# Performance work log

Measured on AMD Instinct MI355X. Metric: run time of the kernel, lower is better.

Reference implementation:

```python
import jax, jax.numpy as jnp
import numpy as np

NF4 = jnp.array([-1.0, -0.6961928009986877, -0.5250730514526367, -0.39491748809814453,
                 -0.28444138169288635, -0.18477343022823334, -0.09105003625154495, 0.0,
                 0.07958029955625534, 0.16093020141124725, 0.24611230194568634,
                 0.33791524171829224, 0.44070982933044434, 0.5626170039176941,
                 0.7229568362236023, 1.0], dtype=jnp.float32)
BLOCK_SIZE = 64
SCALING = 32.0 / 16.0  # alpha / rank


def setup_inputs() -> dict:
    key = jax.random.key(0)
    k = jax.random.split(key, 6)
    B, S, IN, OUT, R = 4, 128, 4096, 11008, 16
    n_blocks = (OUT * IN) // BLOCK_SIZE  # 704512, exact (no padding needed)
    return {
        "x": jax.random.normal(k[0], (B, S, IN), jnp.float32),
        "weight_indices": jax.random.randint(k[1], (OUT, IN), 0, 16, dtype=jnp.int32),
        "weight_scales": jax.random.uniform(k[2], (n_blocks,), jnp.float32),
        "lora_A": jax.random.normal(k[3], (IN, R), jnp.float32),
        "lora_B": jax.random.normal(k[4], (R, OUT), jnp.float32),
        "bias": jax.random.normal(k[5], (OUT,), jnp.float32),
    }


def dequantize_nf4(indices, scales, shape):
    # LUT gather then blockwise absmax scale
    w = NF4[indices.reshape(-1)]                    # [out*in]
    w = w.reshape(-1, BLOCK_SIZE) * scales[:, None]  # [n_blocks, block]
    return w.reshape(shape)                          # [out, in]


def reference(x, weight_indices, weight_scales, lora_A, lora_B, bias):
    W = dequantize_nf4(weight_indices, weight_scales, weight_indices.shape)  # [out, in]
    base = jnp.einsum("bsi,oi->bso", x, W) + bias                            # F.linear
    lora = (x @ lora_A) @ lora_B                                             # low-rank path (dropout p=0 -> identity)
    return base + lora * SCALING
```

## Files before the change

kernel.cpp:

```cpp
#include <hip/hip_runtime.h>
#include <stdint.h>

typedef __bf16 bf16x8 __attribute__((ext_vector_type(8)));
typedef float f32x4 __attribute__((ext_vector_type(4)));
typedef unsigned short ushort_t;

#define N_OUT 11008
#define K_DIM 4096
#define M_DIM 512
#define BM 256
#define BN 64
#define BK 64
#define KHALF 2048
#define NT 32

__constant__ float c_nf4[16] = {
    -1.0f, -0.6961928009986877f, -0.5250730514526367f, -0.39491748809814453f,
    -0.28444138169288635f, -0.18477343022823334f, -0.09105003625154495f, 0.0f,
    0.07958029955625534f, 0.16093020141124725f, 0.24611230194568634f,
    0.33791524171829224f, 0.44070982933044434f, 0.5626170039176941f,
    0.7229568362236023f, 1.0f};

__device__ __forceinline__ uint32_t pkbf(float lo, float hi) {
  uint32_t ul = __builtin_bit_cast(uint32_t, lo);
  uint32_t uh = __builtin_bit_cast(uint32_t, hi);
  return ((ul + 0x8000u) >> 16) | ((uh + 0x8000u) & 0xffff0000u);
}

__device__ __forceinline__ void async16(const void* g, void* l) {
  __builtin_amdgcn_global_load_lds(
      (const __attribute__((address_space(1))) void*)g,
      (__attribute__((address_space(3))) void*)l, 16, 0, 0);
}

__device__ __forceinline__ bf16x8 ldfrag(const ushort_t* p) {
  uint4 r = *reinterpret_cast<const uint4*>(p);
  return __builtin_bit_cast(bf16x8, r);
}

__device__ __forceinline__ uint32_t dq2(int a, int b, float s, const float2* lut) {
  float2 l = lut[a | (b << 4)];
  return pkbf(l.x * s, l.y * s);
}

__global__ void k_prep(const float* __restrict__ x, const float* __restrict__ lA,
                       const float* __restrict__ lB, const float* __restrict__ bias,
                       ushort_t* __restrict__ xbf, ushort_t* __restrict__ xap,
                       ushort_t* __restrict__ btp, float* __restrict__ out) {
  const int b = blockIdx.x, t = threadIdx.x;
  if (b < 1024) {
    int oc = b * 256 + t;
    int m = oc >> 9;
    int cr = oc & 511;
    int win = cr >> 3, cp = cr & 7;
    int c = cp ^ (m & 7);
    const float4* s4 = (const float4*)(x + (size_t)m * K_DIM + win * 64 + c * 8);
    float4 v0 = s4[0], v1 = s4[1];
    uint4 o;
    o.x = pkbf(v0.x, v0.y);
    o.y = pkbf(v0.z, v0.w);
    o.z = pkbf(v1.x, v1.y);
    o.w = pkbf(v1.z, v1.w);
    ((uint4*)xbf)[oc] = o;
  } else if (b < 1536) {
    __shared__ float red[256 * 17];
    int m = b - 1024;
    int ks = t * 16;
    alignas(16) float xs[16];
    const f32x4* xv = (const f32x4*)(x + (size_t)m * K_DIM + ks);
    ((f32x4*)xs)[0] = xv[0];
    ((f32x4*)xs)[1] = xv[1];
    ((f32x4*)xs)[2] = xv[2];
    ((f32x4*)xs)[3] = xv[3];
    f32x4 ac0 = 0.f, ac1 = 0.f, ac2 = 0.f, ac3 = 0.f;
#pragma unroll
    for (int kk = 0; kk < 16; ++kk) {
      float xk = xs[kk];
      const f32x4* l4 = (const f32x4*)(lA + (size_t)(ks + kk) * 16);
      ac0 += xk * l4[0];
      ac1 += xk * l4[1];
      ac2 += xk * l4[2];
      ac3 += xk * l4[3];
    }
#pragma unroll
    for (int r = 0; r < 4; ++r) {
      red[t * 17 + r] = ac0[r];
      red[t * 17 + 4 + r] = ac1[r];
      red[t * 17 + 8 + r] = ac2[r];
      red[t * 17 + 12 + r] = ac3[r];
    }
    __syncthreads();
#pragma unroll
    for (int s = 128; s >= 16; s >>= 1) {
      if (t < s)
        for (int r = 0; r < 16; ++r) red[t * 17 + r] += red[(t + s) * 17 + r];
      __syncthreads();
    }
    if (t < 32) {
      float v = 0.f;
      if (t < 16) {
        for (int p = 0; p < 16; ++p) v += red[p * 17 + t];
        v *= 2.0f;
      }
      uint32_t u = __builtin_bit_cast(uint32_t, v);
      xap[(size_t)m * 32 + t] = (ushort_t)((u + 0x8000u) >> 16);
    }
  } else if (b < 1579) {
    int o = (b - 1536) * 256 + t;
    uint32_t p[8];
#pragma unroll
    for (int j = 0; j < 8; ++j)
      p[j] = pkbf(lB[(size_t)(2 * j) * N_OUT + o], lB[(size_t)(2 * j + 1) * N_OUT + o]);
    uint4* dst = reinterpret_cast<uint4*>(btp + (size_t)o * 32);
    dst[0] = make_uint4(p[0], p[1], p[2], p[3]);
    dst[1] = make_uint4(p[4], p[5], p[6], p[7]);
    dst[2] = make_uint4(0u, 0u, 0u, 0u);
    dst[3] = make_uint4(0u, 0u, 0u, 0u);
  } else {
    int i = (b - 1579) * 256 + t;
    int col4 = i % 2752;
    ((float4*)out)[i] = ((const float4*)bias)[col4];
  }
}

__launch_bounds__(256, 3)
__global__ void k_main(const ushort_t* __restrict__ xbf, const int* __restrict__ wi,
                       const float* __restrict__ sc, const ushort_t* __restrict__ xap,
                       const ushort_t* __restrict__ btp, float* __restrict__ out) {
  __shared__ __align__(16) ushort_t lds_a[BM * BK];
  __shared__ __align__(16) ushort_t lds_b[BN * 72];
  __shared__ float2 lutp[256];

  const int t = threadIdx.x;
  const int lane = t & 63;
  const int w = t >> 6;
  const int o0 = blockIdx.x * BN;
  const int m0 = blockIdx.y * BM;
  const int kh = blockIdx.z;
  const int k0 = kh * KHALF;

  lutp[t] = make_float2(c_nf4[t & 15], c_nf4[t >> 4]);

  const int brow = t >> 2, bq = t & 3;
  const int* gb = wi + (size_t)(o0 + brow) * K_DIM + k0 + bq * 16;
  const float* gs = sc + (size_t)(o0 + brow) * 64 + kh * 32;
  ushort_t* lb = lds_b + brow * 72 + bq * 16;

  const ushort_t* ga =
      xbf + (size_t)(m0 + w * 64 + (lane >> 3)) * K_DIM + k0 + (lane & 7) * 8;
  ushort_t* la_dst = lds_a + w * 4096 + lane * 8;

  f32x4 acc[4][4];
#pragma unroll
  for (int mi = 0; mi < 4; ++mi)
#pragma unroll
    for (int ni = 0; ni < 4; ++ni) acc[mi][ni] = (f32x4){0.f, 0.f, 0.f, 0.f};

  int4 bi0 = ((const int4*)gb)[0], bi1 = ((const int4*)gb)[1];
  int4 bi2 = ((const int4*)gb)[2], bi3 = ((const int4*)gb)[3];
  float s = gs[0];
  gb += BK;
  uint4 braw;

  const ushort_t* afb = lds_a + (w * 64 + (lane & 15)) * BK;
  const int q = lane >> 4;
  const ushort_t* bfb = lds_b + (lane & 15) * 72 + q * 8;

#pragma unroll 1
  for (int kt = 0; kt < NT; ++kt) {
    __syncthreads();
    uint4 w0, w1;
    w0.x = dq2(bi0.x, bi0.y, s, lutp);
    w0.y = dq2(bi0.z, bi0.w, s, lutp);
    w0.z = dq2(bi1.x, bi1.y, s, lutp);
    w0.w = dq2(bi1.z, bi1.w, s, lutp);
    w1.x = dq2(bi2.x, bi2.y, s, lutp);
    w1.y = dq2(bi2.z, bi2.w, s, lutp);
    w1.z = dq2(bi3.x, bi3.y, s, lutp);
    w1.w = dq2(bi3.z, bi3.w, s, lutp);
    *reinterpret_cast<uint4*>(lb) = w0;
    *reinterpret_cast<uint4*>(lb + 8) = w1;
#pragma unroll
    for (int j = 0; j < 8; ++j)
      async16(ga + (size_t)j * 8 * K_DIM + kt * BK, la_dst + j * 512);
    __syncthreads();
    if (kt + 1 < NT) {
      bi0 = ((const int4*)gb)[0];
      bi1 = ((const int4*)gb)[1];
      bi2 = ((const int4*)gb)[2];
      bi3 = ((const int4*)gb)[3];
      s = gs[kt + 1];
      gb += BK;
    } else if (kh == 1) {
      braw = *reinterpret_cast<const uint4*>(btp + (size_t)(o0 + brow) * 32 + bq * 8);
    }
#pragma unroll
    for (int kc = 0; kc < 2; ++kc) {
      const int cpr = ((kc * 4 + q) ^ (lane & 7)) * 8;
      bf16x8 av[4], bv[4];
#pragma unroll
      for (int mi = 0; mi < 4; ++mi) av[mi] = ldfrag(afb + mi * 16 * BK + cpr);
#pragma unroll
      for (int ni = 0; ni < 4; ++ni) bv[ni] = ldfrag(bfb + ni * 16 * 72 + kc * 32);
#pragma unroll
      for (int mi = 0; mi < 4; ++mi)
#pragma unroll
        for (int ni = 0; ni < 4; ++ni)
          acc[mi][ni] = __builtin_amdgcn_mfma_f32_16x16x32_bf16(av[mi], bv[ni],
                                                                acc[mi][ni], 0, 0, 0);
    }
  }

  if (kh == 1) {
    __syncthreads();
    *reinterpret_cast<uint4*>(lds_b + brow * 72 + bq * 8) = braw;
#pragma unroll
    for (int j = 0; j < 4; ++j)
      async16(xap + (size_t)(m0 + w * 64 + j * 16 + (lane >> 2)) * 32 + (lane & 3) * 8,
              lds_a + w * 2048 + j * 512 + lane * 8);
    __syncthreads();
    bf16x8 av[4], bv[4];
#pragma unroll
    for (int mi = 0; mi < 4; ++mi)
      av[mi] = ldfrag(lds_a + w * 2048 + (mi * 16 + (lane & 15)) * 32 + q * 8);
#pragma unroll
    for (int ni = 0; ni < 4; ++ni)
      bv[ni] = ldfrag(lds_b + (ni * 16 + (lane & 15)) * 72 + q * 8);
#pragma unroll
    for (int mi = 0; mi < 4; ++mi)
#pragma unroll
      for (int ni = 0; ni < 4; ++ni)
        acc[mi][ni] = __builtin_amdgcn_mfma_f32_16x16x32_bf16(av[mi], bv[ni],
                                                              acc[mi][ni], 0, 0, 0);
  }

  const int cl = lane & 15, rg = q * 4;
#pragma unroll
  for (int ni = 0; ni < 4; ++ni) {
    int col = o0 + ni * 16 + cl;
#pragma unroll
    for (int mi = 0; mi < 4; ++mi) {
      int row0 = m0 + w * 64 + mi * 16 + rg;
      float* op = out + (size_t)row0 * N_OUT + col;
#pragma unroll
      for (int i = 0; i < 4; ++i) atomicAdd(op + (size_t)i * N_OUT, acc[mi][ni][i]);
    }
  }
}

extern "C" void kernel_launch(void* const* d_in, const int* in_sizes, int n_in,
                              void* d_out, int out_size, void* d_ws, size_t ws_size,
                              hipStream_t stream) {
  const float* x = (const float*)d_in[0];
  const int* wi = (const int*)d_in[1];
  const float* sc = (const float*)d_in[2];
  const float* lA = (const float*)d_in[3];
  const float* lB = (const float*)d_in[4];
  const float* bias = (const float*)d_in[5];
  float* out = (float*)d_out;

  char* wsb = (char*)d_ws;
  ushort_t* xbf = (ushort_t*)wsb;
  ushort_t* xap = (ushort_t*)(wsb + (4u << 20));
  ushort_t* btp = (ushort_t*)(wsb + (4u << 20) + (32u << 10));

  k_prep<<<7083, 256, 0, stream>>>(x, lA, lB, bias, xbf, xap, btp, out);
  dim3 grid(N_OUT / BN, M_DIM / BM, 2);
  k_main<<<grid, 256, 0, stream>>>(xbf, wi, sc, xap, btp, out);
}
```

Baseline: 357.4 us.

## Load activations straight to registers and triple-buffer dequantized weights in LDS

New measurement: 478.4 us. 1.34x slower.

```diff
diff --git a/kernel.cpp b/kernel.cpp
--- a/kernel.cpp
+++ b/kernel.cpp
@@ -13,6 +13,8 @@
 #define BK 64
 #define KHALF 2048
 #define NT 32
+#define LDB 72
+#define BUF (64 * LDB)
 
 __constant__ float c_nf4[16] = {
     -1.0f, -0.6961928009986877f, -0.5250730514526367f, -0.39491748809814453f,
@@ -27,14 +29,12 @@
   return ((ul + 0x8000u) >> 16) | ((uh + 0x8000u) & 0xffff0000u);
 }
 
-__device__ __forceinline__ void async16(const void* g, void* l) {
-  __builtin_amdgcn_global_load_lds(
-      (const __attribute__((address_space(1))) void*)g,
-      (__attribute__((address_space(3))) void*)l, 16, 0, 0);
-}
-
 __device__ __forceinline__ bf16x8 ldfrag(const ushort_t* p) {
   uint4 r = *reinterpret_cast<const uint4*>(p);
+  return __builtin_bit_cast(bf16x8, r);
+}
+
+__device__ __forceinline__ bf16x8 asfrag(uint4 r) {
   return __builtin_bit_cast(bf16x8, r);
 }
 
@@ -47,14 +47,11 @@
                        const float* __restrict__ lB, const float* __restrict__ bias,
                        ushort_t* __restrict__ xbf, ushort_t* __restrict__ xap,
                        ushort_t* __restrict__ btp, float* __restrict__ out) {
+  __shared__ float red[16][17];
   const int b = blockIdx.x, t = threadIdx.x;
   if (b < 1024) {
     int oc = b * 256 + t;
-    int m = oc >> 9;
-    int cr = oc & 511;
-    int win = cr >> 3, cp = cr & 7;
-    int c = cp ^ (m & 7);
-    const float4* s4 = (const float4*)(x + (size_t)m * K_DIM + win * 64 + c * 8);
+    const float4* s4 = reinterpret_cast<const float4*>(x) + (size_t)oc * 2;
     float4 v0 = s4[0], v1 = s4[1];
     uint4 o;
     o.x = pkbf(v0.x, v0.y);
@@ -63,43 +60,19 @@
     o.w = pkbf(v1.z, v1.w);
     ((uint4*)xbf)[oc] = o;
   } else if (b < 1536) {
-    __shared__ float red[256 * 17];
     int m = b - 1024;
-    int ks = t * 16;
-    alignas(16) float xs[16];
-    const f32x4* xv = (const f32x4*)(x + (size_t)m * K_DIM + ks);
-    ((f32x4*)xs)[0] = xv[0];
-    ((f32x4*)xs)[1] = xv[1];
-    ((f32x4*)xs)[2] = xv[2];
-    ((f32x4*)xs)[3] = xv[3];
-    f32x4 ac0 = 0.f, ac1 = 0.f, ac2 = 0.f, ac3 = 0.f;
-#pragma unroll
-    for (int kk = 0; kk < 16; ++kk) {
-      float xk = xs[kk];
-      const f32x4* l4 = (const f32x4*)(lA + (size_t)(ks + kk) * 16);
-      ac0 += xk * l4[0];
-      ac1 += xk * l4[1];
-      ac2 += xk * l4[2];
-      ac3 += xk * l4[3];
-    }
-#pragma unroll
-    for (int r = 0; r < 4; ++r) {
-      red[t * 17 + r] = ac0[r];
-      red[t * 17 + 4 + r] = ac1[r];
-      red[t * 17 + 8 + r] = ac2[r];
-      red[t * 17 + 12 + r] = ac3[r];
-    }
+    int r = t & 15, part = t >> 4;
+    const float* xr = x + (size_t)m * K_DIM + part * 256;
+    const float* ar = lA + (size_t)(part * 256) * 16 + r;
+    float acc = 0.f;
+#pragma unroll 8
+    for (int k = 0; k < 256; ++k) acc += xr[k] * ar[(size_t)k * 16];
+    red[part][r] = acc;
     __syncthreads();
-#pragma unroll
-    for (int s = 128; s >= 16; s >>= 1) {
-      if (t < s)
-        for (int r = 0; r < 16; ++r) red[t * 17 + r] += red[(t + s) * 17 + r];
-      __syncthreads();
-    }
     if (t < 32) {
       float v = 0.f;
       if (t < 16) {
-        for (int p = 0; p < 16; ++p) v += red[p * 17 + t];
+        for (int p = 0; p < 16; ++p) v += red[p][t];
         v *= 2.0f;
       }
       uint32_t u = __builtin_bit_cast(uint32_t, v);
@@ -127,15 +100,15 @@
 __global__ void k_main(const ushort_t* __restrict__ xbf, const int* __restrict__ wi,
                        const float* __restrict__ sc, const ushort_t* __restrict__ xap,
                        const ushort_t* __restrict__ btp, float* __restrict__ out) {
-  __shared__ __align__(16) ushort_t lds_a[BM * BK];
-  __shared__ __align__(16) ushort_t lds_b[BN * 72];
+  __shared__ __align__(16) ushort_t lds_b[3 * BUF];
   __shared__ float2 lutp[256];
 
   const int t = threadIdx.x;
   const int lane = t & 63;
   const int w = t >> 6;
-  const int o0 = blockIdx.x * BN;
-  const int m0 = blockIdx.y * BM;
+  const int q = lane >> 4;
+  const int m0 = blockIdx.x * BM;
+  const int o0 = blockIdx.y * BN;
   const int kh = blockIdx.z;
   const int k0 = kh * KHALF;
 
@@ -144,11 +117,10 @@
   const int brow = t >> 2, bq = t & 3;
   const int* gb = wi + (size_t)(o0 + brow) * K_DIM + k0 + bq * 16;
   const float* gs = sc + (size_t)(o0 + brow) * 64 + kh * 32;
-  ushort_t* lb = lds_b + brow * 72 + bq * 16;
-
-  const ushort_t* ga =
-      xbf + (size_t)(m0 + w * 64 + (lane >> 3)) * K_DIM + k0 + (lane & 7) * 8;
-  ushort_t* la_dst = lds_a + w * 4096 + lane * 8;
+  const int lbo = brow * LDB + bq * 16;
+
+  const ushort_t* gA =
+      xbf + (size_t)(m0 + w * 64 + (lane & 15)) * K_DIM + k0 + q * 8;
 
   f32x4 acc[4][4];
 #pragma unroll
@@ -156,82 +128,115 @@
 #pragma unroll
     for (int ni = 0; ni < 4; ++ni) acc[mi][ni] = (f32x4){0.f, 0.f, 0.f, 0.f};
 
-  int4 bi0 = ((const int4*)gb)[0], bi1 = ((const int4*)gb)[1];
-  int4 bi2 = ((const int4*)gb)[2], bi3 = ((const int4*)gb)[3];
-  float s = gs[0];
-  gb += BK;
-  uint4 braw;
-
-  const ushort_t* afb = lds_a + (w * 64 + (lane & 15)) * BK;
-  const int q = lane >> 4;
-  const ushort_t* bfb = lds_b + (lane & 15) * 72 + q * 8;
-
-#pragma unroll 1
+  int4 bi[2][4];
+  float bs[2];
+  uint4 a_reg[4][2];
+#pragma unroll
+  for (int j = 0; j < 4; ++j) bi[0][j] = reinterpret_cast<const int4*>(gb)[j];
+  bs[0] = gs[0];
+#pragma unroll
+  for (int j = 0; j < 4; ++j) bi[1][j] = reinterpret_cast<const int4*>(gb + 64)[j];
+  bs[1] = gs[1];
+#pragma unroll
+  for (int mi = 0; mi < 4; ++mi)
+#pragma unroll
+    for (int kc = 0; kc < 2; ++kc)
+      a_reg[mi][kc] = *reinterpret_cast<const uint4*>(gA + (size_t)mi * 16 * K_DIM + kc * 32);
+
+  __syncthreads();
+
+  {
+    ushort_t* lb = lds_b + lbo;
+    uint4 w0, w1;
+    w0.x = dq2(bi[0][0].x, bi[0][0].y, bs[0], lutp);
+    w0.y = dq2(bi[0][0].z, bi[0][0].w, bs[0], lutp);
+    w0.z = dq2(bi[0][1].x, bi[0][1].y, bs[0], lutp);
+    w0.w = dq2(bi[0][1].z, bi[0][1].w, bs[0], lutp);
+    w1.x = dq2(bi[0][2].x, bi[0][2].y, bs[0], lutp);
+    w1.y = dq2(bi[0][2].z, bi[0][2].w, bs[0], lutp);
+    w1.z = dq2(bi[0][3].x, bi[0][3].y, bs[0], lutp);
+    w1.w = dq2(bi[0][3].z, bi[0][3].w, bs[0], lutp);
+    *reinterpret_cast<uint4*>(lb) = w0;
+    *reinterpret_cast<uint4*>(lb + 8) = w1;
+  }
+#pragma unroll
+  for (int j = 0; j < 4; ++j) bi[0][j] = reinterpret_cast<const int4*>(gb + 128)[j];
+  bs[0] = gs[2];
+
+  unsigned off_r = 0, off_w = BUF, off_s = 2 * BUF;
+
+#pragma unroll 2
   for (int kt = 0; kt < NT; ++kt) {
     __syncthreads();
-    uint4 w0, w1;
-    w0.x = dq2(bi0.x, bi0.y, s, lutp);
-    w0.y = dq2(bi0.z, bi0.w, s, lutp);
-    w0.z = dq2(bi1.x, bi1.y, s, lutp);
-    w0.w = dq2(bi1.z, bi1.w, s, lutp);
-    w1.x = dq2(bi2.x, bi2.y, s, lutp);
-    w1.y = dq2(bi2.z, bi2.w, s, lutp);
-    w1.z = dq2(bi3.x, bi3.y, s, lutp);
-    w1.w = dq2(bi3.z, bi3.w, s, lutp);
-    *reinterpret_cast<uint4*>(lb) = w0;
-    *reinterpret_cast<uint4*>(lb + 8) = w1;
-#pragma unroll
-    for (int j = 0; j < 8; ++j)
-      async16(ga + (size_t)j * 8 * K_DIM + kt * BK, la_dst + j * 512);
-    __syncthreads();
+    const ushort_t* bb = lds_b + off_r + (lane & 15) * LDB + q * 8;
+    bf16x8 bv0[4], bv1[4];
+#pragma unroll
+    for (int ni = 0; ni < 4; ++ni) bv0[ni] = ldfrag(bb + ni * 16 * LDB);
+#pragma unroll
+    for (int ni = 0; ni < 4; ++ni) bv1[ni] = ldfrag(bb + ni * 16 * LDB + 32);
+    const int ns = (kt + 1) & 1;
     if (kt + 1 < NT) {
-      bi0 = ((const int4*)gb)[0];
-      bi1 = ((const int4*)gb)[1];
-      bi2 = ((const int4*)gb)[2];
-      bi3 = ((const int4*)gb)[3];
-      s = gs[kt + 1];
-      gb += BK;
+      ushort_t* lb = lds_b + off_w + lbo;
+      uint4 w0, w1;
+      w0.x = dq2(bi[ns][0].x, bi[ns][0].y, bs[ns], lutp);
+      w0.y = dq2(bi[ns][0].z, bi[ns][0].w, bs[ns], lutp);
+      w0.z = dq2(bi[ns][1].x, bi[ns][1].y, bs[ns], lutp);
+      w0.w = dq2(bi[ns][1].z, bi[ns][1].w, bs[ns], lutp);
+      w1.x = dq2(bi[ns][2].x, bi[ns][2].y, bs[ns], lutp);
+      w1.y = dq2(bi[ns][2].z, bi[ns][2].w, bs[ns], lutp);
+      w1.z = dq2(bi[ns][3].x, bi[ns][3].y, bs[ns], lutp);
+      w1.w = dq2(bi[ns][3].z, bi[ns][3].w, bs[ns], lutp);
+      *reinterpret_cast<uint4*>(lb) = w0;
+      *reinterpret_cast<uint4*>(lb + 8) = w1;
+    }
+#pragma unroll
+    for (int mi = 0; mi < 4; ++mi)
+#pragma unroll
+      for (int ni = 0; ni < 4; ++ni)
+        acc[mi][ni] = __builtin_amdgcn_mfma_f32_16x16x32_bf16(asfrag(a_reg[mi][0]),
+                                                              bv0[ni], acc[mi][ni], 0, 0, 0);
+#pragma unroll
+    for (int mi = 0; mi < 4; ++mi)
+#pragma unroll
+      for (int ni = 0; ni < 4; ++ni)
+        acc[mi][ni] = __builtin_amdgcn_mfma_f32_16x16x32_bf16(asfrag(a_reg[mi][1]),
+                                                              bv1[ni], acc[mi][ni], 0, 0, 0);
+    if (kt + 3 < NT) {
+      const int4* gp = reinterpret_cast<const int4*>(gb + (size_t)(kt + 3) * 64);
+#pragma unroll
+      for (int j = 0; j < 4; ++j) bi[ns][j] = gp[j];
+      bs[ns] = gs[kt + 3];
+    }
+    if (kt + 1 < NT) {
+#pragma unroll
+      for (int mi = 0; mi < 4; ++mi)
+#pragma unroll
+        for (int kc = 0; kc < 2; ++kc)
+          a_reg[mi][kc] = *reinterpret_cast<const uint4*>(
+              gA + (size_t)mi * 16 * K_DIM + (size_t)(kt + 1) * 64 + kc * 32);
     } else if (kh == 1) {
-      braw = *reinterpret_cast<const uint4*>(btp + (size_t)(o0 + brow) * 32 + bq * 8);
-    }
-#pragma unroll
-    for (int kc = 0; kc < 2; ++kc) {
-      const int cpr = ((kc * 4 + q) ^ (lane & 7)) * 8;
-      bf16x8 av[4], bv[4];
-#pragma unroll
-      for (int mi = 0; mi < 4; ++mi) av[mi] = ldfrag(afb + mi * 16 * BK + cpr);
-#pragma unroll
-      for (int ni = 0; ni < 4; ++ni) bv[ni] = ldfrag(bfb + ni * 16 * 72 + kc * 32);
 #pragma unroll
       for (int mi = 0; mi < 4; ++mi)
-#pragma unroll
-        for (int ni = 0; ni < 4; ++ni)
-          acc[mi][ni] = __builtin_amdgcn_mfma_f32_16x16x32_bf16(av[mi], bv[ni],
-                                                                acc[mi][ni], 0, 0, 0);
-    }
+        a_reg[mi][0] = *reinterpret_cast<const uint4*>(
+            xap + (size_t)(m0 + w * 64 + mi * 16 + (lane & 15)) * 32 + q * 8);
+#pragma unroll
+      for (int ni = 0; ni < 4; ++ni)
+        a_reg[ni][1] = *reinterpret_cast<const uint4*>(
+            btp + (size_t)(o0 + ni * 16 + (lane & 15)) * 32 + q * 8);
+    }
+    unsigned tmp = off_r;
+    off_r = off_w;
+    off_w = off_s;
+    off_s = tmp;
   }
 
   if (kh == 1) {
-    __syncthreads();
-    *reinterpret_cast<uint4*>(lds_b + brow * 72 + bq * 8) = braw;
-#pragma unroll
-    for (int j = 0; j < 4; ++j)
-      async16(xap + (size_t)(m0 + w * 64 + j * 16 + (lane >> 2)) * 32 + (lane & 3) * 8,
-              lds_a + w * 2048 + j * 512 + lane * 8);
-    __syncthreads();
-    bf16x8 av[4], bv[4];
 #pragma unroll
     for (int mi = 0; mi < 4; ++mi)
-      av[mi] = ldfrag(lds_a + w * 2048 + (mi * 16 + (lane & 15)) * 32 + q * 8);
-#pragma unroll
-    for (int ni = 0; ni < 4; ++ni)
-      bv[ni] = ldfrag(lds_b + (ni * 16 + (lane & 15)) * 72 + q * 8);
-#pragma unroll
-    for (int mi = 0; mi < 4; ++mi)
-#pragma unroll
-      for (int ni = 0; ni < 4; ++ni)
-        acc[mi][ni] = __builtin_amdgcn_mfma_f32_16x16x32_bf16(av[mi], bv[ni],
-                                                              acc[mi][ni], 0, 0, 0);
+#pragma unroll
+      for (int ni = 0; ni < 4; ++ni)
+        acc[mi][ni] = __builtin_amdgcn_mfma_f32_16x16x32_bf16(
+            asfrag(a_reg[mi][0]), asfrag(a_reg[ni][1]), acc[mi][ni], 0, 0, 0);
   }
 
   const int cl = lane & 15, rg = q * 4;
@@ -265,6 +270,6 @@
   ushort_t* btp = (ushort_t*)(wsb + (4u << 20) + (32u << 10));
 
   k_prep<<<7083, 256, 0, stream>>>(x, lA, lB, bias, xbf, xap, btp, out);
-  dim3 grid(N_OUT / BN, M_DIM / BM, 2);
+  dim3 grid(M_DIM / BM, N_OUT / BN, 2);
   k_main<<<grid, 256, 0, stream>>>(xbf, wi, sc, xap, btp, out);
 }
```
